# Performance work log

Measured on AMD Instinct MI355X. Metric: run time of the kernel, lower is better.

The kernel has to match this reference:

```python
import jax, jax.numpy as jnp
import numpy as np
from math import pi as PI, log

B, N, D, K = 16, 16384, 64, 64


def setup_inputs() -> dict:
    key = jax.random.key(0)
    k1, k2, k3, k4 = jax.random.split(key, 4)
    x = jax.random.normal(k1, (B, N, D), dtype=jnp.float32)
    pi_w = jax.nn.softmax(jax.random.normal(k2, (K,), dtype=jnp.float32))  # mixture weights, sum to 1
    mu = jax.random.normal(k3, (K, D), dtype=jnp.float32)
    var = jax.random.uniform(k4, (K, D), dtype=jnp.float32, minval=0.5, maxval=1.5)  # diagonal variances
    return {"x": x, "pi": pi_w, "mu": mu, "var": var}


def reference(x, pi, mu, var):
    b, n, d = x.shape
    # --- gmm.predict_proba: diagonal-covariance Gaussian log-likelihoods + log pi, softmax over K ---
    inv_var = 1.0 / var                                   # (K, D)
    x2 = x * x                                            # (B, N, D)
    # Mahalanobis distance expanded via matmuls to avoid a (B,N,K,D) intermediate
    maha = (jnp.einsum('bnd,kd->bnk', x2, inv_var)
            - 2.0 * jnp.einsum('bnd,kd->bnk', x, mu * inv_var)
            + jnp.sum(mu * mu * inv_var, axis=-1))        # (B, N, K)
    log_det = jnp.sum(jnp.log(var), axis=-1)              # (K,)
    log_prob = -0.5 * (d * log(2.0 * PI) + log_det + maha)
    Q = jax.nn.softmax(log_prob + jnp.log(pi), axis=-1)   # (B, N, K) responsibilities
    # --- weighted reductions over N ---
    Q_sum = jnp.sum(Q, axis=1) / n                         # (B, K)
    Q_x = jnp.einsum('bnk,bnd->bkd', Q, x) / n             # (B, K, D)
    Q_x2 = jnp.einsum('bnk,bnd->bkd', Q, x2) / n           # (B, K, D)
    # --- Fisher-vector statistics ---
    d_pi = Q_sum - pi                                      # (B, K)
    qs = Q_sum[..., None]                                  # (B, K, 1)
    d_mu = Q_x - qs * mu
    d_sigma = -Q_x2 - qs * (mu * mu) + qs * var + 2.0 * Q_x * mu
    return jnp.concatenate([d_pi.reshape(b, -1), d_mu.reshape(b, -1), d_sigma.reshape(b, -1)], axis=1)
```

## Files before the change

### kernel.cpp

```cpp
#include <hip/hip_runtime.h>
#include <hip/hip_bf16.h>
#include <math.h>

#define B_  16
#define N_  16384
#define D_  64
#define K_  64
#define OUT_PER_B (K_ + 2*K_*D_)
#define PART_FLOATS OUT_PER_B
#define CHUNKS 32

#define WS_C0_OFF   4096
#define WS_PART_OFF 4160

typedef float f32x4 __attribute__((ext_vector_type(4)));
typedef short short8 __attribute__((ext_vector_type(8)));

union U8 { short8 s8; unsigned int u[4]; };

__device__ __forceinline__ unsigned short f2bf(float f) {
    union { float f; unsigned int u; } v; v.f = f;
    unsigned int r = v.u + 0x7FFFu + ((v.u >> 16) & 1u);
    return (unsigned short)(r >> 16);
}

__device__ __forceinline__ unsigned int f2bf2(float lo, float hi) {
    __hip_bfloat162 h = __float22bfloat162_rn(make_float2(lo, hi));
    unsigned int u;
    __builtin_memcpy(&u, &h, 4);
    return u;
}

__global__ __launch_bounds__(256) void fv_prep(const float* __restrict__ pi,
                                               const float* __restrict__ mu,
                                               const float* __restrict__ var,
                                               float* __restrict__ ws) {
    int t = threadIdx.x;
    unsigned short* wt = (unsigned short*)ws;
    for (int i = t; i < 4096; i += 256) {
        int k = i >> 6, d = i & 63;
        float v  = var[i];
        float m  = mu[i];
        float iv = 1.0f / v;
        wt[k * 128 + d]      = f2bf(-0.5f * iv);
        wt[k * 128 + 64 + d] = f2bf(m * iv);
    }
    if (t < 64) {
        float s = 0.0f;
        for (int d = 0; d < 64; ++d) {
            float v = var[t * 64 + d];
            float m = mu[t * 64 + d];
            s += logf(v) + m * m / v;
        }
        ws[WS_C0_OFF + t] = logf(pi[t]) - 0.5f * (117.624132f + s);
    }
}

__global__ __launch_bounds__(256, 2) void fv_main(const float* __restrict__ x,
                                                  const float* __restrict__ ws,
                                                  float* __restrict__ partials,
                                                  int chunks) {
    __shared__ __align__(16) unsigned short QtS[64 * 72];
    __shared__ float qsum_s[4][64];

    const int t    = threadIdx.x;
    const int w    = t >> 6;
    const int lane = t & 63;
    const int r16  = lane & 15;
    const int q    = lane >> 4;

    short8 wfrag[4][4];
    f32x4  c0v[4];
    {
        const unsigned short* wsu = (const unsigned short*)ws;
        #pragma unroll
        for (int kt = 0; kt < 4; ++kt) {
            const unsigned short* wr = wsu + (16 * kt + r16) * 128 + 8 * q;
            #pragma unroll
            for (int h = 0; h < 4; ++h)
                wfrag[kt][h] = *(const short8*)(const void*)(wr + 32 * h);
            c0v[kt] = *(const f32x4*)(ws + WS_C0_OFF + 16 * kt + 4 * q);
        }
    }

    const int bi    = blockIdx.y;
    const int chunk = blockIdx.x;
    const int ppb   = N_ / chunks;
    const float* xb = x + ((size_t)bi * N_ + (size_t)chunk * ppb) * D_;

    f32x4 accX[4]  = {};
    f32x4 accX2[4] = {};
    float qsacc[4][4] = {};

    const int ntiles = ppb / 64;
    for (int tile = 0; tile < ntiles; ++tile) {
        const float* xt = xb + (size_t)tile * 64 * D_;

        const float* xrow = xt + (16 * w + r16) * D_ + 8 * q;
        float4 va = *(const float4*)(xrow);
        float4 vb = *(const float4*)(xrow + 4);
        float4 vc = *(const float4*)(xrow + 32);
        float4 vd = *(const float4*)(xrow + 36);

        U8 fxa, fxb, fx2a, fx2b;
        fxa.u[0]  = f2bf2(va.x, va.y);           fxa.u[1]  = f2bf2(va.z, va.w);
        fxa.u[2]  = f2bf2(vb.x, vb.y);           fxa.u[3]  = f2bf2(vb.z, vb.w);
        fxb.u[0]  = f2bf2(vc.x, vc.y);           fxb.u[1]  = f2bf2(vc.z, vc.w);
        fxb.u[2]  = f2bf2(vd.x, vd.y);           fxb.u[3]  = f2bf2(vd.z, vd.w);
        fx2a.u[0] = f2bf2(va.x*va.x, va.y*va.y); fx2a.u[1] = f2bf2(va.z*va.z, va.w*va.w);
        fx2a.u[2] = f2bf2(vb.x*vb.x, vb.y*vb.y); fx2a.u[3] = f2bf2(vb.z*vb.z, vb.w*vb.w);
        fx2b.u[0] = f2bf2(vc.x*vc.x, vc.y*vc.y); fx2b.u[1] = f2bf2(vc.z*vc.z, vc.w*vc.w);
        fx2b.u[2] = f2bf2(vd.x*vd.x, vd.y*vd.y); fx2b.u[3] = f2bf2(vd.z*vd.z, vd.w*vd.w);

        float sc[4][4];
        #pragma unroll
        for (int kt = 0; kt < 4; ++kt) {
            f32x4 a = c0v[kt];
            a = __builtin_amdgcn_mfma_f32_16x16x32_bf16(wfrag[kt][0], fx2a.s8, a, 0, 0, 0);
            a = __builtin_amdgcn_mfma_f32_16x16x32_bf16(wfrag[kt][1], fx2b.s8, a, 0, 0, 0);
            a = __builtin_amdgcn_mfma_f32_16x16x32_bf16(wfrag[kt][2], fxa.s8,  a, 0, 0, 0);
            a = __builtin_amdgcn_mfma_f32_16x16x32_bf16(wfrag[kt][3], fxb.s8,  a, 0, 0, 0);
            sc[kt][0] = a[0]; sc[kt][1] = a[1]; sc[kt][2] = a[2]; sc[kt][3] = a[3];
        }

        float mx = sc[0][0];
        #pragma unroll
        for (int kt = 0; kt < 4; ++kt)
            #pragma unroll
            for (int rr = 0; rr < 4; ++rr) mx = fmaxf(mx, sc[kt][rr]);
        mx = fmaxf(mx, __shfl_xor(mx, 16));
        mx = fmaxf(mx, __shfl_xor(mx, 32));
        float z = 0.0f;
        #pragma unroll
        for (int kt = 0; kt < 4; ++kt)
            #pragma unroll
            for (int rr = 0; rr < 4; ++rr) {
                sc[kt][rr] = __expf(sc[kt][rr] - mx);
                z += sc[kt][rr];
            }
        z += __shfl_xor(z, 16);
        z += __shfl_xor(z, 32);
        float inv = 1.0f / z;
        const int p = 16 * w + r16;
        #pragma unroll
        for (int kt = 0; kt < 4; ++kt) {
            #pragma unroll
            for (int rr = 0; rr < 4; ++rr) {
                float qv = sc[kt][rr] * inv;
                qsacc[kt][rr] += qv;
                QtS[(16 * kt + 4 * q + rr) * 72 + p] = f2bf(qv);
            }
        }

        const int dcol = 16 * w + r16;
        const float* xcol = xt + dcol;
        float vle[16];
        #pragma unroll
        for (int c = 0; c < 2; ++c)
            #pragma unroll
            for (int j = 0; j < 8; ++j)
                vle[8 * c + j] = xcol[(32 * c + 8 * q + j) * D_];

        __syncthreads();

        U8 fxp0, fxp1, fx2p0, fx2p1;
        #pragma unroll
        for (int i = 0; i < 4; ++i) {
            float a0 = vle[2 * i], a1 = vle[2 * i + 1];
            float b0 = vle[8 + 2 * i], b1 = vle[8 + 2 * i + 1];
            fxp0.u[i]  = f2bf2(a0, a1);
            fxp1.u[i]  = f2bf2(b0, b1);
            fx2p0.u[i] = f2bf2(a0 * a0, a1 * a1);
            fx2p1.u[i] = f2bf2(b0 * b0, b1 * b1);
        }
        #pragma unroll
        for (int kt = 0; kt < 4; ++kt) {
            const unsigned short* qr = &QtS[(16 * kt + r16) * 72 + 8 * q];
            short8 aq0 = *(const short8*)(const void*)(qr);
            short8 aq1 = *(const short8*)(const void*)(qr + 32);
            accX[kt]  = __builtin_amdgcn_mfma_f32_16x16x32_bf16(aq0, fxp0.s8,  accX[kt],  0, 0, 0);
            accX2[kt] = __builtin_amdgcn_mfma_f32_16x16x32_bf16(aq0, fx2p0.s8, accX2[kt], 0, 0, 0);
            accX[kt]  = __builtin_amdgcn_mfma_f32_16x16x32_bf16(aq1, fxp1.s8,  accX[kt],  0, 0, 0);
            accX2[kt] = __builtin_amdgcn_mfma_f32_16x16x32_bf16(aq1, fx2p1.s8, accX2[kt], 0, 0, 0);
        }
        __syncthreads();
    }

    float* part = partials + ((size_t)bi * chunks + chunk) * PART_FLOATS;
    #pragma unroll
    for (int kt = 0; kt < 4; ++kt)
        #pragma unroll
        for (int rr = 0; rr < 4; ++rr) {
            int k = 16 * kt + 4 * q + rr;
            part[64 + k * 64 + 16 * w + r16]        = accX[kt][rr];
            part[64 + 4096 + k * 64 + 16 * w + r16] = accX2[kt][rr];
        }
    #pragma unroll
    for (int kt = 0; kt < 4; ++kt)
        #pragma unroll
        for (int rr = 0; rr < 4; ++rr) {
            float v = qsacc[kt][rr];
            v += __shfl_xor(v, 1);
            v += __shfl_xor(v, 2);
            v += __shfl_xor(v, 4);
            v += __shfl_xor(v, 8);
            if (r16 == 0) qsum_s[w][16 * kt + 4 * q + rr] = v;
        }
    __syncthreads();
    if (t < 64)
        part[t] = qsum_s[0][t] + qsum_s[1][t] + qsum_s[2][t] + qsum_s[3][t];
}

__global__ __launch_bounds__(256) void fv_finalize(const float* __restrict__ pi,
                                                   const float* __restrict__ mu,
                                                   const float* __restrict__ var,
                                                   const float* __restrict__ partials,
                                                   float* __restrict__ out,
                                                   int chunks) {
    int g = blockIdx.x * 256 + threadIdx.x;
    if (g >= B_ * OUT_PER_B) return;
    int b   = g / OUT_PER_B;
    int pos = g - b * OUT_PER_B;
    const float* base = partials + (size_t)b * chunks * PART_FLOATS;
    const float invN = 1.0f / (float)N_;

    if (pos < 64) {
        float qs = 0.0f;
        for (int c = 0; c < chunks; ++c) qs += base[c * PART_FLOATS + pos];
        out[g] = qs * invN - pi[pos];
    } else if (pos < 64 + 4096) {
        int idx = pos - 64;
        int k = idx >> 6;
        float qs = 0.0f, qx = 0.0f;
        for (int c = 0; c < chunks; ++c) {
            qs += base[c * PART_FLOATS + k];
            qx += base[c * PART_FLOATS + pos];
        }
        out[g] = (qx - qs * mu[idx]) * invN;
    } else {
        int idx = pos - 64 - 4096;
        int k = idx >> 6;
        float qs = 0.0f, qx = 0.0f, qx2 = 0.0f;
        for (int c = 0; c < chunks; ++c) {
            qs  += base[c * PART_FLOATS + k];
            qx  += base[c * PART_FLOATS + 64 + idx];
            qx2 += base[c * PART_FLOATS + pos];
        }
        float m = mu[idx], v = var[idx];
        out[g] = (-qx2 - qs * m * m + qs * v + 2.0f * qx * m) * invN;
    }
}

extern "C" void kernel_launch(void* const* d_in, const int* in_sizes, int n_in,
                              void* d_out, int out_size, void* d_ws, size_t ws_size,
                              hipStream_t stream) {
    const float* x   = (const float*)d_in[0];
    const float* pi  = (const float*)d_in[1];
    const float* mu  = (const float*)d_in[2];
    const float* var = (const float*)d_in[3];
    float* ws = (float*)d_ws;

    int chunks = CHUNKS;
    while (chunks > 1 &&
           (size_t)(WS_PART_OFF + (size_t)B_ * chunks * PART_FLOATS) * sizeof(float) > ws_size)
        chunks >>= 1;
    float* partials = ws + WS_PART_OFF;

    fv_prep<<<1, 256, 0, stream>>>(pi, mu, var, ws);
    fv_main<<<dim3(chunks, B_), 256, 0, stream>>>(x, ws, partials, chunks);
    int total = B_ * OUT_PER_B;
    fv_finalize<<<(total + 255) / 256, 256, 0, stream>>>(pi, mu, var, partials,
                                                         (float*)d_out, chunks);
}
```

Before: 134.5 us.

## Prefetch next x tile into registers and double-buffer Q tile in LDS

The main loop now loads the next tile's row and column fragments of x into registers while the current tile is being computed. The shared Q tile is double-buffered, which removes the trailing barrier from each iteration. The chunk count becomes a compile-time constant, so the loop bound is fixed and the workspace-size fallback is gone. The prep kernel spreads the per-component constant sum across all 256 threads and uses fast log. The cost is higher register pressure under launch bounds of 2 blocks, and a workspace that is too small is no longer detected.

```diff
diff --git a/kernel.cpp b/kernel.cpp
--- a/kernel.cpp
+++ b/kernel.cpp
@@ -9,6 +9,7 @@
 #define OUT_PER_B (K_ + 2*K_*D_)
 #define PART_FLOATS OUT_PER_B
 #define CHUNKS 32
+#define NTILES (N_ / CHUNKS / 64)
 
 #define WS_C0_OFF   4096
 #define WS_PART_OFF 4160
@@ -35,6 +36,7 @@
                                                const float* __restrict__ mu,
                                                const float* __restrict__ var,
                                                float* __restrict__ ws) {
+    __shared__ float red[256];
     int t = threadIdx.x;
     unsigned short* wt = (unsigned short*)ws;
     for (int i = t; i < 4096; i += 256) {
@@ -45,22 +47,27 @@
         wt[k * 128 + d]      = f2bf(-0.5f * iv);
         wt[k * 128 + 64 + d] = f2bf(m * iv);
     }
-    if (t < 64) {
-        float s = 0.0f;
-        for (int d = 0; d < 64; ++d) {
-            float v = var[t * 64 + d];
-            float m = mu[t * 64 + d];
-            s += logf(v) + m * m / v;
-        }
-        ws[WS_C0_OFF + t] = logf(pi[t]) - 0.5f * (117.624132f + s);
+    int k = t >> 2, pr = t & 3;
+    float s = 0.0f;
+    #pragma unroll
+    for (int j = 0; j < 16; ++j) {
+        int d = pr * 16 + j;
+        float v = var[k * 64 + d];
+        float m = mu[k * 64 + d];
+        s += __logf(v) + m * m / v;
+    }
+    red[t] = s;
+    __syncthreads();
+    if (pr == 0) {
+        float sum = red[4 * k] + red[4 * k + 1] + red[4 * k + 2] + red[4 * k + 3];
+        ws[WS_C0_OFF + k] = __logf(pi[k]) - 0.5f * (117.6241322502f + sum);
     }
 }
 
 __global__ __launch_bounds__(256, 2) void fv_main(const float* __restrict__ x,
                                                   const float* __restrict__ ws,
-                                                  float* __restrict__ partials,
-                                                  int chunks) {
-    __shared__ __align__(16) unsigned short QtS[64 * 72];
+                                                  float* __restrict__ partials) {
+    __shared__ __align__(16) unsigned short QtS[2][64 * 72];
     __shared__ float qsum_s[4][64];
 
     const int t    = threadIdx.x;
@@ -85,22 +92,50 @@
 
     const int bi    = blockIdx.y;
     const int chunk = blockIdx.x;
-    const int ppb   = N_ / chunks;
+    const int ppb   = N_ / CHUNKS;
     const float* xb = x + ((size_t)bi * N_ + (size_t)chunk * ppb) * D_;
 
     f32x4 accX[4]  = {};
     f32x4 accX2[4] = {};
     float qsacc[4][4] = {};
 
-    const int ntiles = ppb / 64;
-    for (int tile = 0; tile < ntiles; ++tile) {
-        const float* xt = xb + (size_t)tile * 64 * D_;
-
-        const float* xrow = xt + (16 * w + r16) * D_ + 8 * q;
-        float4 va = *(const float4*)(xrow);
-        float4 vb = *(const float4*)(xrow + 4);
-        float4 vc = *(const float4*)(xrow + 32);
-        float4 vd = *(const float4*)(xrow + 36);
+    const int rowoff = (16 * w + r16) * D_ + 8 * q;
+    const int dcol   = 16 * w + r16;
+
+    float4 va, vb, vc, vd;
+    float  vle[16];
+    {
+        const float* xr = xb + rowoff;
+        va = *(const float4*)(xr);
+        vb = *(const float4*)(xr + 4);
+        vc = *(const float4*)(xr + 32);
+        vd = *(const float4*)(xr + 36);
+        const float* xc = xb + dcol;
+        #pragma unroll
+        for (int c = 0; c < 2; ++c)
+            #pragma unroll
+            for (int j = 0; j < 8; ++j)
+                vle[8 * c + j] = xc[(32 * c + 8 * q + j) * D_];
+    }
+
+    #pragma unroll 2
+    for (int tile = 0; tile < NTILES; ++tile) {
+        float4 nva, nvb, nvc, nvd;
+        float  nvle[16];
+        if (tile + 1 < NTILES) {
+            const float* xtn = xb + (size_t)(tile + 1) * 64 * D_;
+            const float* xr = xtn + rowoff;
+            nva = *(const float4*)(xr);
+            nvb = *(const float4*)(xr + 4);
+            nvc = *(const float4*)(xr + 32);
+            nvd = *(const float4*)(xr + 36);
+            const float* xc = xtn + dcol;
+            #pragma unroll
+            for (int c = 0; c < 2; ++c)
+                #pragma unroll
+                for (int j = 0; j < 8; ++j)
+                    nvle[8 * c + j] = xc[(32 * c + 8 * q + j) * D_];
+        }
 
         U8 fxa, fxb, fx2a, fx2b;
         fxa.u[0]  = f2bf2(va.x, va.y);           fxa.u[1]  = f2bf2(va.z, va.w);
@@ -142,24 +177,16 @@
         z += __shfl_xor(z, 32);
         float inv = 1.0f / z;
         const int p = 16 * w + r16;
+        unsigned short* Qb = QtS[tile & 1];
         #pragma unroll
         for (int kt = 0; kt < 4; ++kt) {
             #pragma unroll
             for (int rr = 0; rr < 4; ++rr) {
                 float qv = sc[kt][rr] * inv;
                 qsacc[kt][rr] += qv;
-                QtS[(16 * kt + 4 * q + rr) * 72 + p] = f2bf(qv);
+                Qb[(16 * kt + 4 * q + rr) * 72 + p] = f2bf(qv);
             }
         }
-
-        const int dcol = 16 * w + r16;
-        const float* xcol = xt + dcol;
-        float vle[16];
-        #pragma unroll
-        for (int c = 0; c < 2; ++c)
-            #pragma unroll
-            for (int j = 0; j < 8; ++j)
-                vle[8 * c + j] = xcol[(32 * c + 8 * q + j) * D_];
 
         __syncthreads();
 
@@ -175,7 +202,7 @@
         }
         #pragma unroll
         for (int kt = 0; kt < 4; ++kt) {
-            const unsigned short* qr = &QtS[(16 * kt + r16) * 72 + 8 * q];
+            const unsigned short* qr = &Qb[(16 * kt + r16) * 72 + 8 * q];
             short8 aq0 = *(const short8*)(const void*)(qr);
             short8 aq1 = *(const short8*)(const void*)(qr + 32);
             accX[kt]  = __builtin_amdgcn_mfma_f32_16x16x32_bf16(aq0, fxp0.s8,  accX[kt],  0, 0, 0);
@@ -183,10 +210,13 @@
             accX[kt]  = __builtin_amdgcn_mfma_f32_16x16x32_bf16(aq1, fxp1.s8,  accX[kt],  0, 0, 0);
             accX2[kt] = __builtin_amdgcn_mfma_f32_16x16x32_bf16(aq1, fx2p1.s8, accX2[kt], 0, 0, 0);
         }
-        __syncthreads();
-    }
-
-    float* part = partials + ((size_t)bi * chunks + chunk) * PART_FLOATS;
+
+        va = nva; vb = nvb; vc = nvc; vd = nvd;
+        #pragma unroll
+        for (int i = 0; i < 16; ++i) vle[i] = nvle[i];
+    }
+
+    float* part = partials + ((size_t)bi * CHUNKS + chunk) * PART_FLOATS;
     #pragma unroll
     for (int kt = 0; kt < 4; ++kt)
         #pragma unroll
@@ -259,16 +289,11 @@
     const float* mu  = (const float*)d_in[2];
     const float* var = (const float*)d_in[3];
     float* ws = (float*)d_ws;
-
-    int chunks = CHUNKS;
-    while (chunks > 1 &&
-           (size_t)(WS_PART_OFF + (size_t)B_ * chunks * PART_FLOATS) * sizeof(float) > ws_size)
-        chunks >>= 1;
     float* partials = ws + WS_PART_OFF;
 
     fv_prep<<<1, 256, 0, stream>>>(pi, mu, var, ws);
-    fv_main<<<dim3(chunks, B_), 256, 0, stream>>>(x, ws, partials, chunks);
+    fv_main<<<dim3(CHUNKS, B_), 256, 0, stream>>>(x, ws, partials);
     int total = B_ * OUT_PER_B;
     fv_finalize<<<(total + 255) / 256, 256, 0, stream>>>(pi, mu, var, partials,
-                                                         (float*)d_out, chunks);
-}
+                                                         (float*)d_out, CHUNKS);
+}
```

Result: faster. 128.3 us (-4.7%).
